# Kernel tuning notes

Hardware: AMD Instinct MI355X
Metric: run time of the kernel (lower is better)

## Reference

```python
import jax, jax.numpy as jnp
import numpy as np

N_HEAD = 16
MASK_PENALTY = 10000.0


def setup_inputs() -> dict:
    key = jax.random.key(0)
    k1, k2, k3 = jax.random.split(key, 3)
    B, S, D = 2, 2048, 1024
    x = jax.random.normal(k1, (B, S, D), dtype=jnp.float32)
    w_attn = jax.random.normal(k2, (D, 3 * D), dtype=jnp.float32) * 0.02
    b_attn = jnp.zeros((3 * D,), dtype=jnp.float32)
    w_proj = jax.random.normal(k3, (D, D), dtype=jnp.float32) * 0.02
    b_proj = jnp.zeros((D,), dtype=jnp.float32)
    return {"x": x, "w_attn": w_attn, "b_attn": b_attn, "w_proj": w_proj, "b_proj": b_proj}


def _split_heads(t, n_head):
    B, S, D = t.shape
    return t.reshape(B, S, n_head, D // n_head).transpose(0, 2, 1, 3)  # [B,H,S,dh]


def reference(x, w_attn, b_attn, w_proj, b_proj):
    B, S, D = x.shape
    qkv = x @ w_attn + b_attn  # fused QKV conv1d: [B,S,3D]
    q, k, v = jnp.split(qkv, 3, axis=2)
    q = _split_heads(q, N_HEAD)
    k = _split_heads(k, N_HEAD)
    v = _split_heads(v, N_HEAD)
    dh = D // N_HEAD
    w = jnp.einsum("bhqd,bhkd->bhqk", q, k) / jnp.sqrt(jnp.asarray(dh, dtype=q.dtype))
    # GPT-2 additive causal mask: w*b - 10000*(1-b)
    i = jnp.arange(S)[:, None]
    j = jnp.arange(S)[None, :]
    b = (i >= j).astype(w.dtype)  # nd == ns here
    w = w * b - MASK_PENALTY * (1.0 - b)
    w = jax.nn.softmax(w, axis=-1)
    a = jnp.einsum("bhqk,bhkd->bhqd", w, v)  # [B,H,S,dh]
    a = a.transpose(0, 2, 1, 3).reshape(B, S, D)  # merge heads
    return a @ w_proj + b_proj
```

## Files before the change

### kernel.cpp

```cpp
#include <hip/hip_runtime.h>
#include <hip/hip_bf16.h>


typedef short short8 __attribute__((ext_vector_type(8)));
typedef float f32x4 __attribute__((ext_vector_type(4)));

__device__ __forceinline__ unsigned short f2b(float f) {
    unsigned int x;
    __builtin_memcpy(&x, &f, 4);
    unsigned int r = x + 0x7FFF + ((x >> 16) & 1);
    return (unsigned short)(r >> 16);
}

__device__ __forceinline__ unsigned int pk2(float a, float b) {
    __hip_bfloat162 h = __float22bfloat162_rn(make_float2(a, b));
    unsigned int u;
    __builtin_memcpy(&u, &h, 4);
    return u;
}

__device__ __forceinline__ void load_lds16(const unsigned short* g, unsigned short* l) {
    __builtin_amdgcn_global_load_lds(
        (const __attribute__((address_space(1))) unsigned int*)g,
        (__attribute__((address_space(3))) unsigned int*)l, 16, 0, 0);
}

__global__ __launch_bounds__(256) void prep(const float* __restrict__ x, unsigned int* __restrict__ xb,
                                            const float* __restrict__ wA, unsigned short* __restrict__ wtA,
                                            const float* __restrict__ wP, unsigned short* __restrict__ wtP) {
    const int bx = blockIdx.x, tid = threadIdx.x;
    if (bx < 4096) {
        int i = (bx * 256 + tid) * 4;
        float4 f = *(const float4*)(x + i);
        uint2 p;
        p.x = (unsigned int)f2b(f.x) | ((unsigned int)f2b(f.y) << 16);
        p.y = (unsigned int)f2b(f.z) | ((unsigned int)f2b(f.w) << 16);
        *(uint2*)(xb + i / 2) = p;
        return;
    }
    __shared__ unsigned short t[32][33];
    const float* in;
    unsigned short* out;
    int R, C, gx, gy;
    if (bx < 7168) { int i = bx - 4096; gx = i % 96; gy = i / 96; in = wA; out = wtA; R = 1024; C = 3072; }
    else           { int i = bx - 7168; gx = i % 32; gy = i / 32; in = wP; out = wtP; R = 1024; C = 1024; }
    const int tx = tid & 31, ty = tid >> 5;
    const int c0 = gx * 32, r0 = gy * 32;
#pragma unroll
    for (int i = 0; i < 4; i++)
        t[ty + i * 8][tx] = f2b(in[(r0 + ty + i * 8) * C + c0 + tx]);
    __syncthreads();
#pragma unroll
    for (int i = 0; i < 4; i++)
        out[(c0 + ty + i * 8) * R + r0 + tx] = t[tx][ty + i * 8];
}

__global__ __launch_bounds__(256) void qkv_gemm(const unsigned short* __restrict__ X,
                                                const unsigned short* __restrict__ WT,
                                                const float* __restrict__ bias,
                                                unsigned short* __restrict__ Qo,
                                                unsigned short* __restrict__ Ko,
                                                unsigned short* __restrict__ Vt) {
    __shared__ __align__(16) unsigned short SM[16384];
    unsigned short* As = SM;
    unsigned short* Bs = SM + 8192;
    const int tid = threadIdx.x;
    const int w = tid >> 6, l = tid & 63, l15 = l & 15, quad = l >> 4;
    const int wr = w >> 1, wc = w & 1;
    const int m0 = blockIdx.y * 128, n0 = blockIdx.x * 128;

    const int sr = w * 16 + (l >> 2);
    const int gch = (l & 3) ^ ((l >> 3) & 3);
    const unsigned short* Asrc = X + (size_t)(m0 + sr) * 1024 + gch * 8;
    const unsigned short* Bsrc = WT + (size_t)(n0 + sr) * 1024 + gch * 8;
    const int rswz = (l15 >> 1) & 3;

    f32x4 acc[4][4];
#pragma unroll
    for (int mt = 0; mt < 4; mt++)
#pragma unroll
        for (int nt = 0; nt < 4; nt++) acc[mt][nt] = (f32x4){0.f, 0.f, 0.f, 0.f};

    load_lds16(Asrc, &As[tid * 8]);
    load_lds16(Asrc + 65536, &As[2048 + tid * 8]);
    load_lds16(Bsrc, &Bs[tid * 8]);
    load_lds16(Bsrc + 65536, &Bs[2048 + tid * 8]);

    for (int k0 = 0; k0 < 1024; k0 += 32) {
        const int c = (k0 >> 5) & 1;
        __syncthreads();
        if (k0 + 32 < 1024) {
            const int pc = 1 - c;
            load_lds16(Asrc + k0 + 32, &As[pc * 4096 + tid * 8]);
            load_lds16(Asrc + 65536 + k0 + 32, &As[pc * 4096 + 2048 + tid * 8]);
            load_lds16(Bsrc + k0 + 32, &Bs[pc * 4096 + tid * 8]);
            load_lds16(Bsrc + 65536 + k0 + 32, &Bs[pc * 4096 + 2048 + tid * 8]);
        }

        short8 af[4], bfr[4];
#pragma unroll
        for (int mt = 0; mt < 4; mt++)
            af[mt] = *(const short8*)&As[c * 4096 + (wr * 64 + mt * 16 + l15) * 32 + ((quad ^ rswz) * 8)];
#pragma unroll
        for (int nt = 0; nt < 4; nt++)
            bfr[nt] = *(const short8*)&Bs[c * 4096 + (wc * 64 + nt * 16 + l15) * 32 + ((quad ^ rswz) * 8)];
#pragma unroll
        for (int mt = 0; mt < 4; mt++)
#pragma unroll
            for (int nt = 0; nt < 4; nt++)
                acc[mt][nt] = __builtin_amdgcn_mfma_f32_16x16x32_bf16(af[mt], bfr[nt], acc[mt][nt], 0, 0, 0);
    }

    const int which = n0 >> 10;
    const int c0 = n0 & 1023;
    float bv[4];
#pragma unroll
    for (int nt = 0; nt < 4; nt++) bv[nt] = bias[n0 + wc * 64 + nt * 16 + l15];

    if (which < 2) {
        const float scale = (which == 1) ? 0.125f : 1.0f;
        unsigned short* dst = (which == 0) ? Qo : Ko;
#pragma unroll
        for (int mt = 0; mt < 4; mt++)
#pragma unroll
            for (int nt = 0; nt < 4; nt++)
#pragma unroll
                for (int r = 0; r < 4; r++) {
                    int mg = m0 + wr * 64 + mt * 16 + quad * 4 + r;
                    int cg = c0 + wc * 64 + nt * 16 + l15;
                    float v = (acc[mt][nt][r] + bv[nt]) * scale;
                    int h = cg >> 6, d = cg & 63;
                    dst[(((size_t)(mg >> 11) * 16 + h) * 2048 + (mg & 2047)) * 64 + d] = f2b(v);
                }
    } else {
        const int b = m0 >> 11, sbase = m0 & 2047, h0 = c0 >> 6;
#pragma unroll
        for (int p = 0; p < 2; p++) {
            __syncthreads();
            if (wc == p) {
#pragma unroll
                for (int mt = 0; mt < 4; mt++)
#pragma unroll
                    for (int nt = 0; nt < 4; nt++)
#pragma unroll
                        for (int r = 0; r < 4; r++) {
                            float v = acc[mt][nt][r] + bv[nt];
                            int d = nt * 16 + l15;
                            int mloc = wr * 64 + mt * 16 + quad * 4 + r;
                            SM[d * 128 + (((mloc >> 4) ^ (d & 7)) << 4) + (mloc & 15)] = f2b(v);
                        }
            }
            __syncthreads();
            const int d = tid >> 2, q4 = tid & 3;
            size_t gb = ((size_t)((b * 16 + h0 + p) * 64 + d)) * 2048 + sbase + q4 * 32;
#pragma unroll
            for (int half = 0; half < 2; half++) {
                int mc = q4 * 2 + half;
                const uint4* s = (const uint4*)&SM[d * 128 + ((mc ^ (d & 7)) << 4)];
                *(uint4*)(Vt + gb + half * 16) = s[0];
                *(uint4*)(Vt + gb + half * 16 + 8) = s[1];
            }
        }
    }
}

__global__ __launch_bounds__(256) void attn_k(const unsigned short* __restrict__ Q,
                                              const unsigned short* __restrict__ K,
                                              const unsigned short* __restrict__ Vt,
                                              unsigned short* __restrict__ Om) {
    __shared__ __align__(16) unsigned short SM[20480];
    unsigned short* Ks0 = SM;
    unsigned short* Vts0 = SM + 8192;
    unsigned short* QP = SM + 16384;

    const int tid = threadIdx.x;
    const int w = tid >> 6, l = tid & 63, l15 = l & 15, quad = l >> 4;
    const int wq = w >> 1, ws = w & 1;
    const int bid = blockIdx.x;
    const int qt = 31 - (bid >> 5);
    const int hb = bid & 31;
    const int q0 = qt * 64;
    const unsigned short* Qb = Q + (size_t)hb * 131072;
    const unsigned short* Kb = K + (size_t)hb * 131072;
    const unsigned short* Vb = Vt + (size_t)hb * 131072;

    const int sr = w * 8 + (l >> 3);
    const int gch = (l & 7) ^ (l >> 3);
    const int swz7 = l15 & 7;

    load_lds16(Qb + (q0 + sr) * 64 + gch * 8, &QP[tid * 8]);
    load_lds16(Qb + (q0 + 32 + sr) * 64 + gch * 8, &QP[2048 + tid * 8]);
    load_lds16(Kb + sr * 64 + gch * 8, &Ks0[tid * 8]);
    load_lds16(Kb + (32 + sr) * 64 + gch * 8, &Ks0[2048 + tid * 8]);
    load_lds16(Vb + sr * 2048 + gch * 8, &Vts0[tid * 8]);
    load_lds16(Vb + (32 + sr) * 2048 + gch * 8, &Vts0[2048 + tid * 8]);
    __syncthreads();

    short8 qf[2][2];
#pragma unroll
    for (int qnt = 0; qnt < 2; qnt++)
#pragma unroll
        for (int ks = 0; ks < 2; ks++)
            qf[qnt][ks] = *(const short8*)&QP[(wq * 32 + qnt * 16 + l15) * 64 + (((ks * 4 + quad) ^ swz7) << 3)];

    short8 ones;
#pragma unroll
    for (int j = 0; j < 8; j++) ones[j] = (short)0x3F80;

    f32x4 o[2][4], lacc[2];
#pragma unroll
    for (int pmt = 0; pmt < 2; pmt++) {
        lacc[pmt] = (f32x4){0.f, 0.f, 0.f, 0.f};
#pragma unroll
        for (int dnt = 0; dnt < 4; dnt++) o[pmt][dnt] = (f32x4){0.f, 0.f, 0.f, 0.f};
    }

    for (int kt = 0; kt <= qt; kt++) {
        const int c = kt & 1;
        const unsigned short* Ksc = Ks0 + c * 4096;
        const unsigned short* Vtsc = Vts0 + c * 4096;
        __syncthreads();
        if (kt < qt) {
            const int kn = (kt + 1) * 64, pc = 1 - c;
            load_lds16(Kb + (kn + sr) * 64 + gch * 8, &Ks0[pc * 4096 + tid * 8]);
            load_lds16(Kb + (kn + 32 + sr) * 64 + gch * 8, &Ks0[pc * 4096 + 2048 + tid * 8]);
            load_lds16(Vb + sr * 2048 + kn + gch * 8, &Vts0[pc * 4096 + tid * 8]);
            load_lds16(Vb + (32 + sr) * 2048 + kn + gch * 8, &Vts0[pc * 4096 + 2048 + tid * 8]);
        }

        f32x4 sa[2][2];
#pragma unroll
        for (int smt = 0; smt < 2; smt++)
#pragma unroll
            for (int qnt = 0; qnt < 2; qnt++) sa[smt][qnt] = (f32x4){0.f, 0.f, 0.f, 0.f};
#pragma unroll
        for (int ks = 0; ks < 2; ks++) {
            short8 kf[2];
#pragma unroll
            for (int smt = 0; smt < 2; smt++)
                kf[smt] = *(const short8*)&Ksc[(ws * 32 + smt * 16 + l15) * 64 + (((ks * 4 + quad) ^ swz7) << 3)];
#pragma unroll
            for (int smt = 0; smt < 2; smt++)
#pragma unroll
                for (int qnt = 0; qnt < 2; qnt++)
                    sa[smt][qnt] = __builtin_amdgcn_mfma_f32_16x16x32_bf16(kf[smt], qf[qnt][ks], sa[smt][qnt], 0, 0, 0);
        }

        float pv[2][2][4];
        if (kt == qt) {
#pragma unroll
            for (int smt = 0; smt < 2; smt++)
#pragma unroll
                for (int qnt = 0; qnt < 2; qnt++)
#pragma unroll
                    for (int r = 0; r < 4; r++) {
                        int cg = kt * 64 + ws * 32 + smt * 16 + quad * 4 + r;
                        int rg = q0 + wq * 32 + qnt * 16 + l15;
                        pv[smt][qnt][r] = (cg <= rg) ? __expf(sa[smt][qnt][r]) : 0.f;
                    }
        } else {
#pragma unroll
            for (int smt = 0; smt < 2; smt++)
#pragma unroll
                for (int qnt = 0; qnt < 2; qnt++)
#pragma unroll
                    for (int r = 0; r < 4; r++)
                        pv[smt][qnt][r] = __expf(sa[smt][qnt][r]);
        }

#pragma unroll
        for (int smt = 0; smt < 2; smt++)
#pragma unroll
            for (int qnt = 0; qnt < 2; qnt++) {
                int q = wq * 32 + qnt * 16 + l15;
                int sb = ws * 32 + smt * 16 + quad * 4;
                int ch = (sb >> 3) ^ (q & 7);
                int a16 = q * 64 + (ch << 3) + (sb & 7);
                uint2 u;
                u.x = pk2(pv[smt][qnt][0], pv[smt][qnt][1]);
                u.y = pk2(pv[smt][qnt][2], pv[smt][qnt][3]);
                *(uint2*)&QP[a16] = u;
            }
        asm volatile("s_waitcnt lgkmcnt(0)" ::: "memory");

        short8 pf[2];
#pragma unroll
        for (int pmt = 0; pmt < 2; pmt++) {
            pf[pmt] = *(const short8*)&QP[(wq * 32 + pmt * 16 + l15) * 64 + (((ws * 4 + quad) ^ swz7) << 3)];
            lacc[pmt] = __builtin_amdgcn_mfma_f32_16x16x32_bf16(pf[pmt], ones, lacc[pmt], 0, 0, 0);
        }
#pragma unroll
        for (int dnt = 0; dnt < 4; dnt++) {
            short8 vf = *(const short8*)&Vtsc[(dnt * 16 + l15) * 64 + (((ws * 4 + quad) ^ swz7) << 3)];
#pragma unroll
            for (int pmt = 0; pmt < 2; pmt++)
                o[pmt][dnt] = __builtin_amdgcn_mfma_f32_16x16x32_bf16(pf[pmt], vf, o[pmt][dnt], 0, 0, 0);
        }
    }

    __syncthreads();
    float* red = (float*)SM;
    float* myp = red + (wq * 64 + l) * 41;
    if (ws == 1) {
#pragma unroll
        for (int pmt = 0; pmt < 2; pmt++) {
#pragma unroll
            for (int dnt = 0; dnt < 4; dnt++)
#pragma unroll
                for (int r = 0; r < 4; r++) myp[pmt * 16 + dnt * 4 + r] = o[pmt][dnt][r];
#pragma unroll
            for (int r = 0; r < 4; r++) myp[32 + pmt * 4 + r] = lacc[pmt][r];
        }
    }
    __syncthreads();
    if (ws == 0) {
        float inv[2][4];
#pragma unroll
        for (int pmt = 0; pmt < 2; pmt++)
#pragma unroll
            for (int r = 0; r < 4; r++)
                inv[pmt][r] = 1.0f / (lacc[pmt][r] + myp[32 + pmt * 4 + r]);
        const int b = hb >> 4, h = hb & 15;
#pragma unroll
        for (int pmt = 0; pmt < 2; pmt++)
#pragma unroll
            for (int dnt = 0; dnt < 4; dnt++)
#pragma unroll
                for (int r = 0; r < 4; r++) {
                    float val = (o[pmt][dnt][r] + myp[pmt * 16 + dnt * 4 + r]) * inv[pmt][r];
                    int sg = q0 + wq * 32 + pmt * 16 + quad * 4 + r;
                    int col = h * 64 + dnt * 16 + l15;
                    Om[((size_t)(b * 2048 + sg)) * 1024 + col] = f2b(val);
                }
    }
}

__global__ __launch_bounds__(256) void proj_gemm(const unsigned short* __restrict__ A,
                                                 const unsigned short* __restrict__ WT,
                                                 const float* __restrict__ bias,
                                                 float* __restrict__ out) {
    __shared__ __align__(16) unsigned short As[2][4096];
    __shared__ __align__(16) unsigned short Bs[2][2048];
    const int tid = threadIdx.x;
    const int w = tid >> 6, l = tid & 63, l15 = l & 15, quad = l >> 4;
    const int wr = w >> 1, wc = w & 1;
    const int m0 = blockIdx.y * 128, n0 = blockIdx.x * 64;

    const int sr = w * 16 + (l >> 2);
    const int gch = (l & 3) ^ ((l >> 3) & 3);
    const unsigned short* Asrc = A + (size_t)(m0 + sr) * 1024 + gch * 8;
    const unsigned short* Bsrc = WT + (size_t)(n0 + sr) * 1024 + gch * 8;
    const int rswz = (l15 >> 1) & 3;

    f32x4 acc[4][2];
#pragma unroll
    for (int mt = 0; mt < 4; mt++)
#pragma unroll
        for (int nt = 0; nt < 2; nt++) acc[mt][nt] = (f32x4){0.f, 0.f, 0.f, 0.f};

    load_lds16(Asrc, &As[0][tid * 8]);
    load_lds16(Asrc + 65536, &As[0][2048 + tid * 8]);
    load_lds16(Bsrc, &Bs[0][tid * 8]);

    for (int k0 = 0; k0 < 1024; k0 += 32) {
        const int c = (k0 >> 5) & 1;
        __syncthreads();
        if (k0 + 32 < 1024) {
            const int pc = 1 - c;
            load_lds16(Asrc + k0 + 32, &As[pc][tid * 8]);
            load_lds16(Asrc + 65536 + k0 + 32, &As[pc][2048 + tid * 8]);
            load_lds16(Bsrc + k0 + 32, &Bs[pc][tid * 8]);
        }

        short8 af[4], bfr[2];
#pragma unroll
        for (int mt = 0; mt < 4; mt++)
            af[mt] = *(const short8*)&As[c][(wr * 64 + mt * 16 + l15) * 32 + ((quad ^ rswz) * 8)];
#pragma unroll
        for (int nt = 0; nt < 2; nt++)
            bfr[nt] = *(const short8*)&Bs[c][(wc * 32 + nt * 16 + l15) * 32 + ((quad ^ rswz) * 8)];
#pragma unroll
        for (int mt = 0; mt < 4; mt++)
#pragma unroll
            for (int nt = 0; nt < 2; nt++)
                acc[mt][nt] = __builtin_amdgcn_mfma_f32_16x16x32_bf16(af[mt], bfr[nt], acc[mt][nt], 0, 0, 0);
    }

#pragma unroll
    for (int mt = 0; mt < 4; mt++)
#pragma unroll
        for (int nt = 0; nt < 2; nt++)
#pragma unroll
            for (int r = 0; r < 4; r++) {
                int mg = m0 + wr * 64 + mt * 16 + quad * 4 + r;
                int ng = n0 + wc * 32 + nt * 16 + l15;
                out[(size_t)mg * 1024 + ng] = acc[mt][nt][r] + bias[ng];
            }
}

extern "C" void kernel_launch(void* const* d_in, const int* in_sizes, int n_in,
                              void* d_out, int out_size, void* d_ws, size_t ws_size,
                              hipStream_t stream) {
    (void)in_sizes; (void)n_in; (void)out_size; (void)ws_size;
    const float* x      = (const float*)d_in[0];
    const float* w_attn = (const float*)d_in[1];
    const float* b_attn = (const float*)d_in[2];
    const float* w_proj = (const float*)d_in[3];
    const float* b_proj = (const float*)d_in[4];
    float* out = (float*)d_out;
    unsigned short* ws = (unsigned short*)d_ws;

    unsigned short* wtA  = ws;
    unsigned short* wtP  = wtA + 3145728;
    unsigned short* Qw   = wtP + 1048576;
    unsigned short* Kw   = Qw + 4194304;
    unsigned short* Vtw  = Kw + 4194304;
    unsigned short* XbOm = Vtw + 4194304;

    prep<<<8192, 256, 0, stream>>>(x, (unsigned int*)XbOm, w_attn, wtA, w_proj, wtP);
    qkv_gemm<<<dim3(24, 32), 256, 0, stream>>>(XbOm, wtA, b_attn, Qw, Kw, Vtw);
    attn_k<<<1024, 256, 0, stream>>>(Qw, Kw, Vtw, XbOm);
    proj_gemm<<<dim3(16, 32), 256, 0, stream>>>(XbOm, wtP, b_proj, out);
}
```

Measured before the change: 171.9 us.

## Pair causal query tiles per attention block and widen weight-prep transpose tiles

Each attention block now handles two query tiles, a long one (31-pi) and a short one (pi), so every block does the same total causal work. Grid size halves to 512 and the tail imbalance across blocks should go away. The prep kernel moves to 64x64 transpose tiles with float4 loads and 16-byte stores, and each block converts four float4 chunks of x, cutting block count and giving wider memory accesses. In exchange, each attention block runs its two tiles one after the other, which lowers parallelism and adds a sync and a reload between them.

```diff
diff --git a/kernel.cpp b/kernel.cpp
--- a/kernel.cpp
+++ b/kernel.cpp
@@ -29,30 +29,41 @@
                                             const float* __restrict__ wA, unsigned short* __restrict__ wtA,
                                             const float* __restrict__ wP, unsigned short* __restrict__ wtP) {
     const int bx = blockIdx.x, tid = threadIdx.x;
-    if (bx < 4096) {
-        int i = (bx * 256 + tid) * 4;
-        float4 f = *(const float4*)(x + i);
-        uint2 p;
-        p.x = (unsigned int)f2b(f.x) | ((unsigned int)f2b(f.y) << 16);
-        p.y = (unsigned int)f2b(f.z) | ((unsigned int)f2b(f.w) << 16);
-        *(uint2*)(xb + i / 2) = p;
+    if (bx < 1024) {
+#pragma unroll
+        for (int j = 0; j < 4; j++) {
+            int i = (bx * 1024 + j * 256 + tid) * 4;
+            float4 f = *(const float4*)(x + i);
+            uint2 p;
+            p.x = pk2(f.x, f.y);
+            p.y = pk2(f.z, f.w);
+            *(uint2*)(xb + i / 2) = p;
+        }
         return;
     }
-    __shared__ unsigned short t[32][33];
+    __shared__ unsigned short T[64][72];
     const float* in;
     unsigned short* out;
-    int R, C, gx, gy;
-    if (bx < 7168) { int i = bx - 4096; gx = i % 96; gy = i / 96; in = wA; out = wtA; R = 1024; C = 3072; }
-    else           { int i = bx - 7168; gx = i % 32; gy = i / 32; in = wP; out = wtP; R = 1024; C = 1024; }
-    const int tx = tid & 31, ty = tid >> 5;
-    const int c0 = gx * 32, r0 = gy * 32;
-#pragma unroll
-    for (int i = 0; i < 4; i++)
-        t[ty + i * 8][tx] = f2b(in[(r0 + ty + i * 8) * C + c0 + tx]);
+    int R, C, r0, c0;
+    if (bx < 1792) { int t = bx - 1024; c0 = (t % 48) * 64; r0 = (t / 48) * 64; in = wA; out = wtA; R = 1024; C = 3072; }
+    else           { int t = bx - 1792; c0 = (t % 16) * 64; r0 = (t / 16) * 64; in = wP; out = wtP; R = 1024; C = 1024; }
+    const int ty = tid >> 4, tx = tid & 15;
+#pragma unroll
+    for (int i = 0; i < 4; i++) {
+        int row = ty + i * 16;
+        float4 f = *(const float4*)(in + (size_t)(r0 + row) * C + c0 + tx * 4);
+        T[tx * 4 + 0][row] = f2b(f.x);
+        T[tx * 4 + 1][row] = f2b(f.y);
+        T[tx * 4 + 2][row] = f2b(f.z);
+        T[tx * 4 + 3][row] = f2b(f.w);
+    }
     __syncthreads();
-#pragma unroll
-    for (int i = 0; i < 4; i++)
-        out[(c0 + ty + i * 8) * R + r0 + tx] = t[tx][ty + i * 8];
+    const int c = tid >> 2, rq = tid & 3;
+    const uint4* s = (const uint4*)&T[c][rq * 16];
+    uint4 a = s[0], b = s[1];
+    unsigned short* dst = out + (size_t)(c0 + c) * R + r0 + rq * 16;
+    *(uint4*)dst = a;
+    *(uint4*)(dst + 8) = b;
 }
 
 __global__ __launch_bounds__(256) void qkv_gemm(const unsigned short* __restrict__ X,
@@ -177,9 +188,8 @@
     const int w = tid >> 6, l = tid & 63, l15 = l & 15, quad = l >> 4;
     const int wq = w >> 1, ws = w & 1;
     const int bid = blockIdx.x;
-    const int qt = 31 - (bid >> 5);
+    const int pi = bid >> 5;
     const int hb = bid & 31;
-    const int q0 = qt * 64;
     const unsigned short* Qb = Q + (size_t)hb * 131072;
     const unsigned short* Kb = K + (size_t)hb * 131072;
     const unsigned short* Vb = Vt + (size_t)hb * 131072;
@@ -187,151 +197,158 @@
     const int sr = w * 8 + (l >> 3);
     const int gch = (l & 7) ^ (l >> 3);
     const int swz7 = l15 & 7;
-
-    load_lds16(Qb + (q0 + sr) * 64 + gch * 8, &QP[tid * 8]);
-    load_lds16(Qb + (q0 + 32 + sr) * 64 + gch * 8, &QP[2048 + tid * 8]);
-    load_lds16(Kb + sr * 64 + gch * 8, &Ks0[tid * 8]);
-    load_lds16(Kb + (32 + sr) * 64 + gch * 8, &Ks0[2048 + tid * 8]);
-    load_lds16(Vb + sr * 2048 + gch * 8, &Vts0[tid * 8]);
-    load_lds16(Vb + (32 + sr) * 2048 + gch * 8, &Vts0[2048 + tid * 8]);
-    __syncthreads();
-
-    short8 qf[2][2];
-#pragma unroll
-    for (int qnt = 0; qnt < 2; qnt++)
-#pragma unroll
-        for (int ks = 0; ks < 2; ks++)
-            qf[qnt][ks] = *(const short8*)&QP[(wq * 32 + qnt * 16 + l15) * 64 + (((ks * 4 + quad) ^ swz7) << 3)];
+    const int b = hb >> 4, h = hb & 15;
 
     short8 ones;
 #pragma unroll
     for (int j = 0; j < 8; j++) ones[j] = (short)0x3F80;
 
-    f32x4 o[2][4], lacc[2];
-#pragma unroll
-    for (int pmt = 0; pmt < 2; pmt++) {
-        lacc[pmt] = (f32x4){0.f, 0.f, 0.f, 0.f};
-#pragma unroll
-        for (int dnt = 0; dnt < 4; dnt++) o[pmt][dnt] = (f32x4){0.f, 0.f, 0.f, 0.f};
-    }
-
-    for (int kt = 0; kt <= qt; kt++) {
-        const int c = kt & 1;
-        const unsigned short* Ksc = Ks0 + c * 4096;
-        const unsigned short* Vtsc = Vts0 + c * 4096;
+    for (int half = 0; half < 2; half++) {
+        const int qt = half ? pi : (31 - pi);
+        const int q0 = qt * 64;
+
+        if (half) __syncthreads();
+
+        load_lds16(Qb + (q0 + sr) * 64 + gch * 8, &QP[tid * 8]);
+        load_lds16(Qb + (q0 + 32 + sr) * 64 + gch * 8, &QP[2048 + tid * 8]);
+        load_lds16(Kb + sr * 64 + gch * 8, &Ks0[tid * 8]);
+        load_lds16(Kb + (32 + sr) * 64 + gch * 8, &Ks0[2048 + tid * 8]);
+        load_lds16(Vb + sr * 2048 + gch * 8, &Vts0[tid * 8]);
+        load_lds16(Vb + (32 + sr) * 2048 + gch * 8, &Vts0[2048 + tid * 8]);
         __syncthreads();
-        if (kt < qt) {
-            const int kn = (kt + 1) * 64, pc = 1 - c;
-            load_lds16(Kb + (kn + sr) * 64 + gch * 8, &Ks0[pc * 4096 + tid * 8]);
-            load_lds16(Kb + (kn + 32 + sr) * 64 + gch * 8, &Ks0[pc * 4096 + 2048 + tid * 8]);
-            load_lds16(Vb + sr * 2048 + kn + gch * 8, &Vts0[pc * 4096 + tid * 8]);
-            load_lds16(Vb + (32 + sr) * 2048 + kn + gch * 8, &Vts0[pc * 4096 + 2048 + tid * 8]);
-        }
-
-        f32x4 sa[2][2];
-#pragma unroll
-        for (int smt = 0; smt < 2; smt++)
-#pragma unroll
-            for (int qnt = 0; qnt < 2; qnt++) sa[smt][qnt] = (f32x4){0.f, 0.f, 0.f, 0.f};
-#pragma unroll
-        for (int ks = 0; ks < 2; ks++) {
-            short8 kf[2];
+
+        short8 qf[2][2];
+#pragma unroll
+        for (int qnt = 0; qnt < 2; qnt++)
+#pragma unroll
+            for (int ks = 0; ks < 2; ks++)
+                qf[qnt][ks] = *(const short8*)&QP[(wq * 32 + qnt * 16 + l15) * 64 + (((ks * 4 + quad) ^ swz7) << 3)];
+
+        f32x4 o[2][4], lacc[2];
+#pragma unroll
+        for (int pmt = 0; pmt < 2; pmt++) {
+            lacc[pmt] = (f32x4){0.f, 0.f, 0.f, 0.f};
+#pragma unroll
+            for (int dnt = 0; dnt < 4; dnt++) o[pmt][dnt] = (f32x4){0.f, 0.f, 0.f, 0.f};
+        }
+
+        for (int kt = 0; kt <= qt; kt++) {
+            const int c = kt & 1;
+            const unsigned short* Ksc = Ks0 + c * 4096;
+            const unsigned short* Vtsc = Vts0 + c * 4096;
+            __syncthreads();
+            if (kt < qt) {
+                const int kn = (kt + 1) * 64, pc = 1 - c;
+                load_lds16(Kb + (kn + sr) * 64 + gch * 8, &Ks0[pc * 4096 + tid * 8]);
+                load_lds16(Kb + (kn + 32 + sr) * 64 + gch * 8, &Ks0[pc * 4096 + 2048 + tid * 8]);
+                load_lds16(Vb + sr * 2048 + kn + gch * 8, &Vts0[pc * 4096 + tid * 8]);
+                load_lds16(Vb + (32 + sr) * 2048 + kn + gch * 8, &Vts0[pc * 4096 + 2048 + tid * 8]);
+            }
+
+            f32x4 sa[2][2];
 #pragma unroll
             for (int smt = 0; smt < 2; smt++)
-                kf[smt] = *(const short8*)&Ksc[(ws * 32 + smt * 16 + l15) * 64 + (((ks * 4 + quad) ^ swz7) << 3)];
+#pragma unroll
+                for (int qnt = 0; qnt < 2; qnt++) sa[smt][qnt] = (f32x4){0.f, 0.f, 0.f, 0.f};
+#pragma unroll
+            for (int ks = 0; ks < 2; ks++) {
+                short8 kf[2];
+#pragma unroll
+                for (int smt = 0; smt < 2; smt++)
+                    kf[smt] = *(const short8*)&Ksc[(ws * 32 + smt * 16 + l15) * 64 + (((ks * 4 + quad) ^ swz7) << 3)];
+#pragma unroll
+                for (int smt = 0; smt < 2; smt++)
+#pragma unroll
+                    for (int qnt = 0; qnt < 2; qnt++)
+                        sa[smt][qnt] = __builtin_amdgcn_mfma_f32_16x16x32_bf16(kf[smt], qf[qnt][ks], sa[smt][qnt], 0, 0, 0);
+            }
+
+            float pv[2][2][4];
+            if (kt == qt) {
+#pragma unroll
+                for (int smt = 0; smt < 2; smt++)
+#pragma unroll
+                    for (int qnt = 0; qnt < 2; qnt++)
+#pragma unroll
+                        for (int r = 0; r < 4; r++) {
+                            int cg = kt * 64 + ws * 32 + smt * 16 + quad * 4 + r;
+                            int rg = q0 + wq * 32 + qnt * 16 + l15;
+                            pv[smt][qnt][r] = (cg <= rg) ? __expf(sa[smt][qnt][r]) : 0.f;
+                        }
+            } else {
+#pragma unroll
+                for (int smt = 0; smt < 2; smt++)
+#pragma unroll
+                    for (int qnt = 0; qnt < 2; qnt++)
+#pragma unroll
+                        for (int r = 0; r < 4; r++)
+                            pv[smt][qnt][r] = __expf(sa[smt][qnt][r]);
+            }
+
 #pragma unroll
             for (int smt = 0; smt < 2; smt++)
 #pragma unroll
-                for (int qnt = 0; qnt < 2; qnt++)
-                    sa[smt][qnt] = __builtin_amdgcn_mfma_f32_16x16x32_bf16(kf[smt], qf[qnt][ks], sa[smt][qnt], 0, 0, 0);
-        }
-
-        float pv[2][2][4];
-        if (kt == qt) {
-#pragma unroll
-            for (int smt = 0; smt < 2; smt++)
-#pragma unroll
-                for (int qnt = 0; qnt < 2; qnt++)
+                for (int qnt = 0; qnt < 2; qnt++) {
+                    int q = wq * 32 + qnt * 16 + l15;
+                    int sb = ws * 32 + smt * 16 + quad * 4;
+                    int ch = (sb >> 3) ^ (q & 7);
+                    int a16 = q * 64 + (ch << 3) + (sb & 7);
+                    uint2 u;
+                    u.x = pk2(pv[smt][qnt][0], pv[smt][qnt][1]);
+                    u.y = pk2(pv[smt][qnt][2], pv[smt][qnt][3]);
+                    *(uint2*)&QP[a16] = u;
+                }
+            asm volatile("s_waitcnt lgkmcnt(0)" ::: "memory");
+
+            short8 pf[2];
+#pragma unroll
+            for (int pmt = 0; pmt < 2; pmt++) {
+                pf[pmt] = *(const short8*)&QP[(wq * 32 + pmt * 16 + l15) * 64 + (((ws * 4 + quad) ^ swz7) << 3)];
+                lacc[pmt] = __builtin_amdgcn_mfma_f32_16x16x32_bf16(pf[pmt], ones, lacc[pmt], 0, 0, 0);
+            }
+#pragma unroll
+            for (int dnt = 0; dnt < 4; dnt++) {
+                short8 vf = *(const short8*)&Vtsc[(dnt * 16 + l15) * 64 + (((ws * 4 + quad) ^ swz7) << 3)];
+#pragma unroll
+                for (int pmt = 0; pmt < 2; pmt++)
+                    o[pmt][dnt] = __builtin_amdgcn_mfma_f32_16x16x32_bf16(pf[pmt], vf, o[pmt][dnt], 0, 0, 0);
+            }
+        }
+
+        __syncthreads();
+        float* red = (float*)SM;
+        float* myp = red + (wq * 64 + l) * 41;
+        if (ws == 1) {
+#pragma unroll
+            for (int pmt = 0; pmt < 2; pmt++) {
+#pragma unroll
+                for (int dnt = 0; dnt < 4; dnt++)
+#pragma unroll
+                    for (int r = 0; r < 4; r++) myp[pmt * 16 + dnt * 4 + r] = o[pmt][dnt][r];
+#pragma unroll
+                for (int r = 0; r < 4; r++) myp[32 + pmt * 4 + r] = lacc[pmt][r];
+            }
+        }
+        __syncthreads();
+        if (ws == 0) {
+            float inv[2][4];
+#pragma unroll
+            for (int pmt = 0; pmt < 2; pmt++)
+#pragma unroll
+                for (int r = 0; r < 4; r++)
+                    inv[pmt][r] = 1.0f / (lacc[pmt][r] + myp[32 + pmt * 4 + r]);
+#pragma unroll
+            for (int pmt = 0; pmt < 2; pmt++)
+#pragma unroll
+                for (int dnt = 0; dnt < 4; dnt++)
 #pragma unroll
                     for (int r = 0; r < 4; r++) {
-                        int cg = kt * 64 + ws * 32 + smt * 16 + quad * 4 + r;
-                        int rg = q0 + wq * 32 + qnt * 16 + l15;
-                        pv[smt][qnt][r] = (cg <= rg) ? __expf(sa[smt][qnt][r]) : 0.f;
+                        float val = (o[pmt][dnt][r] + myp[pmt * 16 + dnt * 4 + r]) * inv[pmt][r];
+                        int sg = q0 + wq * 32 + pmt * 16 + quad * 4 + r;
+                        int col = h * 64 + dnt * 16 + l15;
+                        Om[((size_t)(b * 2048 + sg)) * 1024 + col] = f2b(val);
                     }
-        } else {
-#pragma unroll
-            for (int smt = 0; smt < 2; smt++)
-#pragma unroll
-                for (int qnt = 0; qnt < 2; qnt++)
-#pragma unroll
-                    for (int r = 0; r < 4; r++)
-                        pv[smt][qnt][r] = __expf(sa[smt][qnt][r]);
-        }
-
-#pragma unroll
-        for (int smt = 0; smt < 2; smt++)
-#pragma unroll
-            for (int qnt = 0; qnt < 2; qnt++) {
-                int q = wq * 32 + qnt * 16 + l15;
-                int sb = ws * 32 + smt * 16 + quad * 4;
-                int ch = (sb >> 3) ^ (q & 7);
-                int a16 = q * 64 + (ch << 3) + (sb & 7);
-                uint2 u;
-                u.x = pk2(pv[smt][qnt][0], pv[smt][qnt][1]);
-                u.y = pk2(pv[smt][qnt][2], pv[smt][qnt][3]);
-                *(uint2*)&QP[a16] = u;
-            }
-        asm volatile("s_waitcnt lgkmcnt(0)" ::: "memory");
-
-        short8 pf[2];
-#pragma unroll
-        for (int pmt = 0; pmt < 2; pmt++) {
-            pf[pmt] = *(const short8*)&QP[(wq * 32 + pmt * 16 + l15) * 64 + (((ws * 4 + quad) ^ swz7) << 3)];
-            lacc[pmt] = __builtin_amdgcn_mfma_f32_16x16x32_bf16(pf[pmt], ones, lacc[pmt], 0, 0, 0);
-        }
-#pragma unroll
-        for (int dnt = 0; dnt < 4; dnt++) {
-            short8 vf = *(const short8*)&Vtsc[(dnt * 16 + l15) * 64 + (((ws * 4 + quad) ^ swz7) << 3)];
-#pragma unroll
-            for (int pmt = 0; pmt < 2; pmt++)
-                o[pmt][dnt] = __builtin_amdgcn_mfma_f32_16x16x32_bf16(pf[pmt], vf, o[pmt][dnt], 0, 0, 0);
-        }
-    }
-
-    __syncthreads();
-    float* red = (float*)SM;
-    float* myp = red + (wq * 64 + l) * 41;
-    if (ws == 1) {
-#pragma unroll
-        for (int pmt = 0; pmt < 2; pmt++) {
-#pragma unroll
-            for (int dnt = 0; dnt < 4; dnt++)
-#pragma unroll
-                for (int r = 0; r < 4; r++) myp[pmt * 16 + dnt * 4 + r] = o[pmt][dnt][r];
-#pragma unroll
-            for (int r = 0; r < 4; r++) myp[32 + pmt * 4 + r] = lacc[pmt][r];
-        }
-    }
-    __syncthreads();
-    if (ws == 0) {
-        float inv[2][4];
-#pragma unroll
-        for (int pmt = 0; pmt < 2; pmt++)
-#pragma unroll
-            for (int r = 0; r < 4; r++)
-                inv[pmt][r] = 1.0f / (lacc[pmt][r] + myp[32 + pmt * 4 + r]);
-        const int b = hb >> 4, h = hb & 15;
-#pragma unroll
-        for (int pmt = 0; pmt < 2; pmt++)
-#pragma unroll
-            for (int dnt = 0; dnt < 4; dnt++)
-#pragma unroll
-                for (int r = 0; r < 4; r++) {
-                    float val = (o[pmt][dnt][r] + myp[pmt * 16 + dnt * 4 + r]) * inv[pmt][r];
-                    int sg = q0 + wq * 32 + pmt * 16 + quad * 4 + r;
-                    int col = h * 64 + dnt * 16 + l15;
-                    Om[((size_t)(b * 2048 + sg)) * 1024 + col] = f2b(val);
-                }
+        }
     }
 }
 
@@ -417,8 +434,8 @@
     unsigned short* Vtw  = Kw + 4194304;
     unsigned short* XbOm = Vtw + 4194304;
 
-    prep<<<8192, 256, 0, stream>>>(x, (unsigned int*)XbOm, w_attn, wtA, w_proj, wtP);
+    prep<<<2048, 256, 0, stream>>>(x, (unsigned int*)XbOm, w_attn, wtA, w_proj, wtP);
     qkv_gemm<<<dim3(24, 32), 256, 0, stream>>>(XbOm, wtA, b_attn, Qw, Kw, Vtw);
-    attn_k<<<1024, 256, 0, stream>>>(Qw, Kw, Vtw, XbOm);
+    attn_k<<<512, 256, 0, stream>>>(Qw, Kw, Vtw, XbOm);
     proj_gemm<<<dim3(16, 32), 256, 0, stream>>>(XbOm, wtP, b_proj, out);
 }
```

After: 176.5 us. 2.7% more time.
